# Kernel optimization log

Hardware: AMD Instinct MI355X
Metric: run time of the kernel (lower is better)

The kernel has to match this reference:

```python
import jax, jax.numpy as jnp
import numpy as np

N_NODES = 100000
N_EDGES = 1600000
D_IN = 256
D_OUT = 128


def setup_inputs() -> dict:
    key = jax.random.key(0)
    k1, k2, k3, k4, k5, k6 = jax.random.split(key, 6)
    inp = {
        "input": jax.random.normal(k1, (N_NODES, D_IN), dtype=jnp.float32),
        "edge_row": jax.random.randint(k2, (N_EDGES,), 0, N_NODES),
        "edge_col": jax.random.randint(k3, (N_EDGES,), 0, N_NODES),
        "edge_val": jax.random.uniform(k4, (N_EDGES,), dtype=jnp.float32),
        "W": jax.random.normal(k5, (D_IN, D_OUT), dtype=jnp.float32) * (1.0 / np.sqrt(D_IN)),
        "b": jax.random.normal(k6, (D_OUT,), dtype=jnp.float32) * 0.01,
    }
    return inp


def reference(input, edge_row, edge_col, edge_val, W, b):
    # support = Linear(input)  -> [N, D_OUT]
    support = jnp.dot(input, W) + b
    # sparse.mm(adj, support): out[r] = sum_e val[e] * support[col[e]] for edges with row[e]==r
    msgs = edge_val[:, None] * support[edge_col]  # [E, D_OUT]
    agg = jax.ops.segment_sum(msgs, edge_row, num_segments=N_NODES)  # [N, D_OUT]
    return jnp.tanh(agg)
```

## Files before the change

### kernel.cpp

```cpp
#include <hip/hip_runtime.h>
#include <math.h>

#define N_NODES 100000
#define N_EDGES 1600000
#define D_IN 256
#define D_OUT 128

#define OFF_SUPPORT 0
#define OFF_COUNTS  51200000
#define OFF_CSREV   51600008
#define OFF_BSUMS   64400008
#define OFF_WTHI    64400416
#define OFF_WTLO    64465952

#define SCAN_CHUNK  1024
#define SCAN_BLOCKS ((N_NODES + SCAN_CHUNK - 1) / SCAN_CHUNK)

#define GB 128
#define GEMM_BLOCKS ((N_NODES + GB - 1) / GB)
#define EDGE_BLOCKS ((N_EDGES + 255) / 256)

#define AP 40

typedef __attribute__((ext_vector_type(8))) short s8v;
typedef __attribute__((ext_vector_type(4))) float f4v;

__device__ __forceinline__ short f2bf(float x) {
  unsigned u = __float_as_uint(x);
  unsigned r = u + 0x7FFF + ((u >> 16) & 1);
  return (short)(r >> 16);
}
__device__ __forceinline__ float bf2f(short h) {
  return __uint_as_float(((unsigned)(unsigned short)h) << 16);
}

__global__ __launch_bounds__(256) void wconv_kernel(
    const float* __restrict__ W, short* __restrict__ wt_hi,
    short* __restrict__ wt_lo) {
  int idx = blockIdx.x * 256 + threadIdx.x;
  int k = idx >> 7;
  int n = idx & 127;
  float v = W[idx];
  short h = f2bf(v);
  wt_hi[n * 256 + k] = h;
  wt_lo[n * 256 + k] = f2bf(v - bf2f(h));
}

__device__ __forceinline__ void gemm_body(
    int gb, const float* __restrict__ input, const short* __restrict__ wt_hi,
    const short* __restrict__ wt_lo, const float* __restrict__ b,
    float* __restrict__ support) {
  __shared__ short Ahi[GB * AP];
  __shared__ short Alo[GB * AP];
  __shared__ short Bhi[D_OUT * AP];
  __shared__ short Blo[D_OUT * AP];

  const int t = threadIdx.x;
  const int node0 = gb * GB;
  const int lane = t & 63;
  const int wv = t >> 6;
  const int qm = lane & 15;
  const int quad = lane >> 4;

  f4v acc[2][8];
#pragma unroll
  for (int mt = 0; mt < 2; mt++)
#pragma unroll
    for (int nt = 0; nt < 8; nt++) acc[mt][nt] = (f4v){0.f, 0.f, 0.f, 0.f};

  for (int k0 = 0; k0 < D_IN; k0 += 32) {
#pragma unroll
    for (int j = 0; j < 4; j++) {
      int i = t + j * 256;
      int row = i >> 3;
      int kf = (i & 7) << 2;
      int node = node0 + row;
      float4 v = make_float4(0.f, 0.f, 0.f, 0.f);
      if (node < N_NODES)
        v = *(const float4*)(input + (size_t)node * D_IN + k0 + kf);
      short4 h, l;
      h.x = f2bf(v.x); l.x = f2bf(v.x - bf2f(h.x));
      h.y = f2bf(v.y); l.y = f2bf(v.y - bf2f(h.y));
      h.z = f2bf(v.z); l.z = f2bf(v.z - bf2f(h.z));
      h.w = f2bf(v.w); l.w = f2bf(v.w - bf2f(h.w));
      *(short4*)&Ahi[row * AP + kf] = h;
      *(short4*)&Alo[row * AP + kf] = l;
    }
#pragma unroll
    for (int j = 0; j < 2; j++) {
      int i = t + j * 256;
      int n = i >> 2;
      int kq = (i & 3) << 3;
      *(s8v*)&Bhi[n * AP + kq] = *(const s8v*)&wt_hi[n * 256 + k0 + kq];
      *(s8v*)&Blo[n * AP + kq] = *(const s8v*)&wt_lo[n * 256 + k0 + kq];
    }
    __syncthreads();

    s8v ah0 = *(s8v*)&Ahi[(wv * 32 + qm) * AP + quad * 8];
    s8v al0 = *(s8v*)&Alo[(wv * 32 + qm) * AP + quad * 8];
    s8v ah1 = *(s8v*)&Ahi[(wv * 32 + 16 + qm) * AP + quad * 8];
    s8v al1 = *(s8v*)&Alo[(wv * 32 + 16 + qm) * AP + quad * 8];
#pragma unroll
    for (int nt = 0; nt < 8; nt++) {
      s8v bh = *(s8v*)&Bhi[(nt * 16 + qm) * AP + quad * 8];
      s8v bl = *(s8v*)&Blo[(nt * 16 + qm) * AP + quad * 8];
      acc[0][nt] = __builtin_amdgcn_mfma_f32_16x16x32_bf16(ah0, bh, acc[0][nt], 0, 0, 0);
      acc[0][nt] = __builtin_amdgcn_mfma_f32_16x16x32_bf16(ah0, bl, acc[0][nt], 0, 0, 0);
      acc[0][nt] = __builtin_amdgcn_mfma_f32_16x16x32_bf16(al0, bh, acc[0][nt], 0, 0, 0);
      acc[1][nt] = __builtin_amdgcn_mfma_f32_16x16x32_bf16(ah1, bh, acc[1][nt], 0, 0, 0);
      acc[1][nt] = __builtin_amdgcn_mfma_f32_16x16x32_bf16(ah1, bl, acc[1][nt], 0, 0, 0);
      acc[1][nt] = __builtin_amdgcn_mfma_f32_16x16x32_bf16(al1, bh, acc[1][nt], 0, 0, 0);
    }
    __syncthreads();
  }

  float bias[8];
#pragma unroll
  for (int nt = 0; nt < 8; nt++) bias[nt] = b[nt * 16 + qm];
#pragma unroll
  for (int mt = 0; mt < 2; mt++) {
#pragma unroll
    for (int nt = 0; nt < 8; nt++) {
      int col = nt * 16 + qm;
#pragma unroll
      for (int r = 0; r < 4; r++) {
        int node = node0 + wv * 32 + mt * 16 + quad * 4 + r;
        if (node < N_NODES)
          support[(size_t)node * D_OUT + col] = acc[mt][nt][r] + bias[nt];
      }
    }
  }
}

__global__ __launch_bounds__(256) void gemm_hist_kernel(
    const float* __restrict__ input, const short* __restrict__ wt_hi,
    const short* __restrict__ wt_lo, const float* __restrict__ b,
    float* __restrict__ support, const int* __restrict__ erow,
    int* __restrict__ counts, int* __restrict__ pos_e) {
  if (blockIdx.x < GEMM_BLOCKS) {
    gemm_body(blockIdx.x, input, wt_hi, wt_lo, b, support);
  } else {
    int e = (blockIdx.x - GEMM_BLOCKS) * 256 + threadIdx.x;
    if (e < N_EDGES) pos_e[e] = atomicAdd(&counts[erow[e]], 1);
  }
}

__global__ __launch_bounds__(256) void build_kernel(
    const int* __restrict__ erow, const int* __restrict__ ecol,
    const float* __restrict__ eval, const int* __restrict__ offsets,
    const int* __restrict__ pos_e, int2* __restrict__ csr_ev) {
  int e = blockIdx.x * 256 + threadIdx.x;
  if (e < N_EDGES) {
    int idx = offsets[erow[e]] + pos_e[e];
    csr_ev[idx] = make_int2(ecol[e], __float_as_int(eval[e]));
  }
}

__global__ __launch_bounds__(256) void scan_phase1(const int* __restrict__ counts,
                                                   int* __restrict__ bsums) {
  __shared__ int ts[256];
  int t = threadIdx.x;
  int idx0 = blockIdx.x * SCAN_CHUNK + t * 4;
  int s = 0;
#pragma unroll
  for (int i = 0; i < 4; i++)
    if (idx0 + i < N_NODES) s += counts[idx0 + i];
  ts[t] = s;
  __syncthreads();
#pragma unroll
  for (int off = 128; off > 0; off >>= 1) {
    if (t < off) ts[t] += ts[t + off];
    __syncthreads();
  }
  if (t == 0) bsums[blockIdx.x] = ts[0];
}

__global__ __launch_bounds__(128) void scan_phase2(int* __restrict__ bsums) {
  __shared__ int s[128];
  int t = threadIdx.x;
  int v = (t < SCAN_BLOCKS) ? bsums[t] : 0;
  s[t] = v;
  __syncthreads();
#pragma unroll
  for (int off = 1; off < 128; off <<= 1) {
    int x = (t >= off) ? s[t - off] : 0;
    __syncthreads();
    s[t] += x;
    __syncthreads();
  }
  if (t < SCAN_BLOCKS) bsums[t] = s[t] - v;
}

__global__ __launch_bounds__(256) void scan_phase3(int* __restrict__ counts,
                                                   const int* __restrict__ bsums) {
  __shared__ int ts[256];
  int t = threadIdx.x;
  int b = blockIdx.x;
  int idx0 = b * SCAN_CHUNK + t * 4;
  int v[4];
  int s = 0;
#pragma unroll
  for (int i = 0; i < 4; i++) {
    v[i] = (idx0 + i < N_NODES) ? counts[idx0 + i] : 0;
    s += v[i];
  }
  ts[t] = s;
  __syncthreads();
#pragma unroll
  for (int off = 1; off < 256; off <<= 1) {
    int x = (t >= off) ? ts[t - off] : 0;
    __syncthreads();
    ts[t] += x;
    __syncthreads();
  }
  int run = bsums[b] + ts[t] - s;
#pragma unroll
  for (int i = 0; i < 4; i++) {
    int idx = idx0 + i;
    if (idx < N_NODES) counts[idx] = run;
    run += v[i];
  }
  if (b == 0 && t == 0) counts[N_NODES] = N_EDGES;
}

__global__ __launch_bounds__(128) void agg_kernel(
    const int* __restrict__ offsets, const int2* __restrict__ csr_ev,
    const float* __restrict__ support, float* __restrict__ out) {
  int r = blockIdx.x;
  int f = threadIdx.x;
  int beg = offsets[r];
  int end = offsets[r + 1];
  float acc = 0.f;
  int j = beg;
  for (; j + 8 <= end; j += 8) {
    int2 e[8];
    float s[8];
#pragma unroll
    for (int u = 0; u < 8; u++) e[u] = csr_ev[j + u];
#pragma unroll
    for (int u = 0; u < 8; u++) s[u] = support[(size_t)e[u].x * D_OUT + f];
#pragma unroll
    for (int u = 0; u < 8; u++) acc = fmaf(__int_as_float(e[u].y), s[u], acc);
  }
  for (; j < end; j++) {
    int2 ev = csr_ev[j];
    acc = fmaf(__int_as_float(ev.y), support[(size_t)ev.x * D_OUT + f], acc);
  }
  out[(size_t)r * D_OUT + f] = tanhf(acc);
}

extern "C" void kernel_launch(void* const* d_in, const int* in_sizes, int n_in,
                              void* d_out, int out_size, void* d_ws, size_t ws_size,
                              hipStream_t stream) {
  const float* input = (const float*)d_in[0];
  const int* erow = (const int*)d_in[1];
  const int* ecol = (const int*)d_in[2];
  const float* eval = (const float*)d_in[3];
  const float* W = (const float*)d_in[4];
  const float* b = (const float*)d_in[5];
  float* out = (float*)d_out;

  char* ws = (char*)d_ws;
  float* support = (float*)(ws + OFF_SUPPORT);
  int* counts = (int*)(ws + OFF_COUNTS);
  int2* csr_ev = (int2*)(ws + OFF_CSREV);
  int* bsums = (int*)(ws + OFF_BSUMS);
  short* wt_hi = (short*)(ws + OFF_WTHI);
  short* wt_lo = (short*)(ws + OFF_WTLO);
  int* pos_e = (int*)d_out;

  hipLaunchKernelGGL(wconv_kernel, dim3((D_IN * D_OUT) / 256), dim3(256), 0,
                     stream, W, wt_hi, wt_lo);
  hipMemsetAsync(ws + OFF_COUNTS, 0, (size_t)(N_NODES + 1) * 4, stream);

  hipLaunchKernelGGL(gemm_hist_kernel, dim3(GEMM_BLOCKS + EDGE_BLOCKS),
                     dim3(256), 0, stream, input, wt_hi, wt_lo, b, support,
                     erow, counts, pos_e);
  hipLaunchKernelGGL(scan_phase1, dim3(SCAN_BLOCKS), dim3(256), 0, stream,
                     counts, bsums);
  hipLaunchKernelGGL(scan_phase2, dim3(1), dim3(128), 0, stream, bsums);
  hipLaunchKernelGGL(scan_phase3, dim3(SCAN_BLOCKS), dim3(256), 0, stream,
                     counts, bsums);
  hipLaunchKernelGGL(build_kernel, dim3(EDGE_BLOCKS), dim3(256), 0, stream,
                     erow, ecol, eval, counts, pos_e, csr_ev);
  hipLaunchKernelGGL(agg_kernel, dim3(N_NODES), dim3(128), 0, stream, counts,
                     csr_ev, support, out);
}
```

Before: 423.9 us.

## Load GEMM fragments directly from global and vectorize aggregation with warp-per-row

```diff
diff --git a/kernel.cpp b/kernel.cpp
--- a/kernel.cpp
+++ b/kernel.cpp
@@ -20,8 +20,6 @@
 #define GEMM_BLOCKS ((N_NODES + GB - 1) / GB)
 #define EDGE_BLOCKS ((N_EDGES + 255) / 256)
 
-#define AP 40
-
 typedef __attribute__((ext_vector_type(8))) short s8v;
 typedef __attribute__((ext_vector_type(4))) float f4v;
 
@@ -32,6 +30,16 @@
 }
 __device__ __forceinline__ float bf2f(short h) {
   return __uint_as_float(((unsigned)(unsigned short)h) << 16);
+}
+
+__device__ __forceinline__ void cvt8(float4 a, float4 b, s8v& h, s8v& l) {
+  float f[8] = {a.x, a.y, a.z, a.w, b.x, b.y, b.z, b.w};
+#pragma unroll
+  for (int i = 0; i < 8; i++) {
+    short hh = f2bf(f[i]);
+    h[i] = hh;
+    l[i] = f2bf(f[i] - bf2f(hh));
+  }
 }
 
 __global__ __launch_bounds__(256) void wconv_kernel(
@@ -50,17 +58,19 @@
     int gb, const float* __restrict__ input, const short* __restrict__ wt_hi,
     const short* __restrict__ wt_lo, const float* __restrict__ b,
     float* __restrict__ support) {
-  __shared__ short Ahi[GB * AP];
-  __shared__ short Alo[GB * AP];
-  __shared__ short Bhi[D_OUT * AP];
-  __shared__ short Blo[D_OUT * AP];
-
   const int t = threadIdx.x;
-  const int node0 = gb * GB;
   const int lane = t & 63;
   const int wv = t >> 6;
   const int qm = lane & 15;
   const int quad = lane >> 4;
+  const int node0 = gb * GB;
+
+  const int row0 = node0 + wv * 32 + qm;
+  const int row1 = row0 + 16;
+  const bool ok0 = row0 < N_NODES;
+  const bool ok1 = row1 < N_NODES;
+  const float* a0p = input + (size_t)row0 * D_IN + quad * 8;
+  const float* a1p = input + (size_t)row1 * D_IN + quad * 8;
 
   f4v acc[2][8];
 #pragma unroll
@@ -69,41 +79,26 @@
     for (int nt = 0; nt < 8; nt++) acc[mt][nt] = (f4v){0.f, 0.f, 0.f, 0.f};
 
   for (int k0 = 0; k0 < D_IN; k0 += 32) {
-#pragma unroll
-    for (int j = 0; j < 4; j++) {
-      int i = t + j * 256;
-      int row = i >> 3;
-      int kf = (i & 7) << 2;
-      int node = node0 + row;
-      float4 v = make_float4(0.f, 0.f, 0.f, 0.f);
-      if (node < N_NODES)
-        v = *(const float4*)(input + (size_t)node * D_IN + k0 + kf);
-      short4 h, l;
-      h.x = f2bf(v.x); l.x = f2bf(v.x - bf2f(h.x));
-      h.y = f2bf(v.y); l.y = f2bf(v.y - bf2f(h.y));
-      h.z = f2bf(v.z); l.z = f2bf(v.z - bf2f(h.z));
-      h.w = f2bf(v.w); l.w = f2bf(v.w - bf2f(h.w));
-      *(short4*)&Ahi[row * AP + kf] = h;
-      *(short4*)&Alo[row * AP + kf] = l;
-    }
-#pragma unroll
-    for (int j = 0; j < 2; j++) {
-      int i = t + j * 256;
-      int n = i >> 2;
-      int kq = (i & 3) << 3;
-      *(s8v*)&Bhi[n * AP + kq] = *(const s8v*)&wt_hi[n * 256 + k0 + kq];
-      *(s8v*)&Blo[n * AP + kq] = *(const s8v*)&wt_lo[n * 256 + k0 + kq];
-    }
-    __syncthreads();
-
-    s8v ah0 = *(s8v*)&Ahi[(wv * 32 + qm) * AP + quad * 8];
-    s8v al0 = *(s8v*)&Alo[(wv * 32 + qm) * AP + quad * 8];
-    s8v ah1 = *(s8v*)&Ahi[(wv * 32 + 16 + qm) * AP + quad * 8];
-    s8v al1 = *(s8v*)&Alo[(wv * 32 + 16 + qm) * AP + quad * 8];
+    float4 z = make_float4(0.f, 0.f, 0.f, 0.f);
+    float4 v00 = z, v01 = z, v10 = z, v11 = z;
+    if (ok0) {
+      v00 = *(const float4*)(a0p + k0);
+      v01 = *(const float4*)(a0p + k0 + 4);
+    }
+    if (ok1) {
+      v10 = *(const float4*)(a1p + k0);
+      v11 = *(const float4*)(a1p + k0 + 4);
+    }
+    s8v ah0, al0, ah1, al1;
+    cvt8(v00, v01, ah0, al0);
+    cvt8(v10, v11, ah1, al1);
+
+    const int koff = k0 + quad * 8;
 #pragma unroll
     for (int nt = 0; nt < 8; nt++) {
-      s8v bh = *(s8v*)&Bhi[(nt * 16 + qm) * AP + quad * 8];
-      s8v bl = *(s8v*)&Blo[(nt * 16 + qm) * AP + quad * 8];
+      const size_t bo = (size_t)(nt * 16 + qm) * 256 + koff;
+      s8v bh = *(const s8v*)(wt_hi + bo);
+      s8v bl = *(const s8v*)(wt_lo + bo);
       acc[0][nt] = __builtin_amdgcn_mfma_f32_16x16x32_bf16(ah0, bh, acc[0][nt], 0, 0, 0);
       acc[0][nt] = __builtin_amdgcn_mfma_f32_16x16x32_bf16(ah0, bl, acc[0][nt], 0, 0, 0);
       acc[0][nt] = __builtin_amdgcn_mfma_f32_16x16x32_bf16(al0, bh, acc[0][nt], 0, 0, 0);
@@ -111,7 +106,6 @@
       acc[1][nt] = __builtin_amdgcn_mfma_f32_16x16x32_bf16(ah1, bl, acc[1][nt], 0, 0, 0);
       acc[1][nt] = __builtin_amdgcn_mfma_f32_16x16x32_bf16(al1, bh, acc[1][nt], 0, 0, 0);
     }
-    __syncthreads();
   }
 
   float bias[8];
@@ -223,30 +217,43 @@
   if (b == 0 && t == 0) counts[N_NODES] = N_EDGES;
 }
 
-__global__ __launch_bounds__(128) void agg_kernel(
+__global__ __launch_bounds__(256) void agg_kernel(
     const int* __restrict__ offsets, const int2* __restrict__ csr_ev,
     const float* __restrict__ support, float* __restrict__ out) {
-  int r = blockIdx.x;
-  int f = threadIdx.x;
+  int r = blockIdx.x * 8 + (threadIdx.x >> 5);
+  int l4 = (threadIdx.x & 31) * 4;
   int beg = offsets[r];
   int end = offsets[r + 1];
-  float acc = 0.f;
+  float4 acc = make_float4(0.f, 0.f, 0.f, 0.f);
   int j = beg;
   for (; j + 8 <= end; j += 8) {
     int2 e[8];
-    float s[8];
+    float4 s[8];
 #pragma unroll
     for (int u = 0; u < 8; u++) e[u] = csr_ev[j + u];
 #pragma unroll
-    for (int u = 0; u < 8; u++) s[u] = support[(size_t)e[u].x * D_OUT + f];
-#pragma unroll
-    for (int u = 0; u < 8; u++) acc = fmaf(__int_as_float(e[u].y), s[u], acc);
+    for (int u = 0; u < 8; u++)
+      s[u] = *(const float4*)(support + (size_t)e[u].x * D_OUT + l4);
+#pragma unroll
+    for (int u = 0; u < 8; u++) {
+      float v = __int_as_float(e[u].y);
+      acc.x = fmaf(v, s[u].x, acc.x);
+      acc.y = fmaf(v, s[u].y, acc.y);
+      acc.z = fmaf(v, s[u].z, acc.z);
+      acc.w = fmaf(v, s[u].w, acc.w);
+    }
   }
   for (; j < end; j++) {
     int2 ev = csr_ev[j];
-    acc = fmaf(__int_as_float(ev.y), support[(size_t)ev.x * D_OUT + f], acc);
-  }
-  out[(size_t)r * D_OUT + f] = tanhf(acc);
+    float4 s = *(const float4*)(support + (size_t)ev.x * D_OUT + l4);
+    float v = __int_as_float(ev.y);
+    acc.x = fmaf(v, s.x, acc.x);
+    acc.y = fmaf(v, s.y, acc.y);
+    acc.z = fmaf(v, s.z, acc.z);
+    acc.w = fmaf(v, s.w, acc.w);
+  }
+  *(float4*)(out + (size_t)r * D_OUT + l4) =
+      make_float4(tanhf(acc.x), tanhf(acc.y), tanhf(acc.z), tanhf(acc.w));
 }
 
 extern "C" void kernel_launch(void* const* d_in, const int* in_sizes, int n_in,
@@ -283,6 +290,6 @@
                      counts, bsums);
   hipLaunchKernelGGL(build_kernel, dim3(EDGE_BLOCKS), dim3(256), 0, stream,
                      erow, ecol, eval, counts, pos_e, csr_ev);
-  hipLaunchKernelGGL(agg_kernel, dim3(N_NODES), dim3(128), 0, stream, counts,
-                     csr_ev, support, out);
-}
+  hipLaunchKernelGGL(agg_kernel, dim3(N_NODES / 8), dim3(256), 0, stream,
+                     counts, csr_ev, support, out);
+}
```

Result: slower. 447.3 us (+5.5%).
